# Kernel tuning notes

Measured on AMD Instinct MI355X. Metric: run time of the kernel, lower is better.

The kernel has to match this reference:

```python
import jax, jax.numpy as jnp
import numpy as np

N, NR, NR_SO = 16, 300, 300
C, NUM_REL = 150, 50
D_PRO, D_ROI, D_REL = 512, 12544, 256
K, R, MAX_RECALL, IOU_THRES = 10, 3, 100, 0.5


def _rand_boxes(key, shape):
    # valid (x1,y1,x2,y2) boxes in an ~1000px image
    k1, k2, k3, k4 = jax.random.split(key, 4)
    x1 = jax.random.uniform(k1, shape) * 800.0
    y1 = jax.random.uniform(k2, shape) * 800.0
    w = jax.random.uniform(k3, shape) * 200.0 + 8.0
    h = jax.random.uniform(k4, shape) * 200.0 + 8.0
    return jnp.stack([x1, y1, x1 + w, y1 + h], -1).astype(jnp.float32)


def setup_inputs() -> dict:
    key = jax.random.key(0)
    ks = jax.random.split(key, 12)
    return {
        "auxiliary_rel": jax.random.normal(ks[0], (N, NR, 2 * D_REL), jnp.float32),
        "class_logits": jax.random.normal(ks[1], (N, 2 * NR, C), jnp.float32),
        "pred_bboxes": _rand_boxes(ks[2], (N, 2 * NR)),
        "pro_features": jax.random.normal(ks[3], (N, NR, D_PRO), jnp.float32),
        "roi_features": jax.random.normal(ks[4], (N, NR, D_ROI), jnp.float32),
        "so_class_logits": jax.random.normal(ks[5], (N, NR_SO, 2 * C), jnp.float32),
        "pred_bboxes_so": _rand_boxes(ks[6], (N, 2 * NR_SO)).reshape(N, NR_SO, 8),
        "so_pro_features": jax.random.normal(ks[7], (N, NR_SO, D_PRO), jnp.float32),
        "so_roi_features": jax.random.normal(ks[8], (N, NR_SO, D_ROI), jnp.float32),
        "rel_logits": jax.random.normal(ks[9], (N, NR_SO, NUM_REL), jnp.float32),
        "rel_feat": jax.random.normal(ks[10], (N, NR_SO, D_REL), jnp.float32),
        "vis_table": jnp.zeros((N, NR), dtype=bool),
    }


def _batch_box_iou(b1, b2):
    # b1: [B,N,4], b2: [B,M,4] -> iou [B,N,M] (+1 area convention as in torch src)
    a1 = (b1[..., 3] - b1[..., 1] + 1.0) * (b1[..., 2] - b1[..., 0] + 1.0)
    a2 = (b2[..., 3] - b2[..., 1] + 1.0) * (b2[..., 2] - b2[..., 0] + 1.0)
    lt = jnp.maximum(b1[:, :, None, :2], b2[:, None, :, :2])
    rb = jnp.minimum(b1[:, :, None, 2:], b2[:, None, :, 2:])
    wh = jnp.clip(rb - lt, 0.0)
    inter = wh[..., 0] * wh[..., 1]
    return inter / (a1[:, :, None] + a2[:, None, :] - inter)


def _swap_so(x):
    # swap subject/object halves of the last dim: view (n,k,2,d/2), flip dim 2
    n, k, d = x.shape
    return x.reshape(n, k, 2, d // 2)[:, :, ::-1, :].reshape(n, k, d)


def _forward(auxiliary_rel, class_logits, pred_bboxes, pro_features, roi_features,
             so_class_logits, pred_bboxes_so, so_pro_features, so_roi_features,
             rel_logits, rel_feat, vis_table):
    n = class_logits.shape[0]
    nr = class_logits.shape[1] // 2
    nr_so = so_pro_features.shape[1]
    # ---------- extend_and_select_tri ----------
    probs = jax.nn.sigmoid(so_class_logits).reshape(n, 2 * nr_so, -1)
    boxes = pred_bboxes_so.reshape(n, 2 * nr_so, 4)
    s_score, s_class = jax.lax.top_k(probs[:, 0::2], R)
    o_score, o_class = jax.lax.top_k(probs[:, 1::2], R)
    X, Y = np.meshgrid(np.arange(R), np.arange(R), indexing='ij')
    X, Y = X.ravel(), Y.ravel()
    R2 = R * R
    score_d = jnp.stack([s_score[:, :, X], o_score[:, :, Y]], -1)  # [n,nr_so,R2,2]
    class_d = jnp.stack([s_class[:, :, X], o_class[:, :, Y]], -1)
    sb = jnp.broadcast_to(boxes[:, 0::2][:, :, None, :], (n, nr_so, R2, 4))
    ob = jnp.broadcast_to(boxes[:, 1::2][:, :, None, :], (n, nr_so, R2, 4))
    boxes_d = jnp.stack([sb, ob], 3).reshape(n, nr_so * R2, 8)
    rel_max = jnp.max(jax.nn.sigmoid(rel_logits), -1)  # [n,nr_so]
    triple = (rel_max[:, :, None] * score_d[..., 0] * score_d[..., 1]).reshape(n, nr_so * R2)
    _, tri_idx = jax.lax.top_k(triple, MAX_RECALL)
    tri_idx = jnp.sort(tri_idx, -1)  # boolean-mask gather returns ascending index order
    sel_class = jnp.take_along_axis(class_d.reshape(n, nr_so * R2, 2), tri_idx[..., None], 1).reshape(n, 1, 2 * MAX_RECALL)
    sel_boxes = jnp.take_along_axis(boxes_d, tri_idx[..., None], 1).reshape(n, 2 * MAX_RECALL, 4)
    # ---------- auxiliary_branch (subject slice) ----------
    cls_s = class_logits[:, 0::2, :]
    box_s = pred_bboxes[:, 0::2, :]
    iou_hit = _batch_box_iou(box_s, sel_boxes) >= IOU_THRES  # [n,nr,2*MR]
    pure = jax.nn.sigmoid(cls_s)
    pure_class = jnp.argmax(pure, -1).astype(jnp.int32)  # topk k=1
    cls_eq = pure_class[:, :, None] == sel_class
    is_new = ~jnp.any(iou_hit & cls_eq, -1)  # [n,nr]
    score = jnp.max(pure, -1) - 2.0 * (~is_new) - 2.0 * vis_table
    _, ent_idx = jax.lax.top_k(score, K)
    ent_idx = jnp.sort(ent_idx, -1)
    new_mask = jnp.zeros((n, nr), dtype=bool).at[jnp.arange(n)[:, None], ent_idx].set(True)
    vis_out = vis_table | new_mask
    take = lambda a: jnp.take_along_axis(a, ent_idx[..., None], 1)
    # ---------- assemble auxiliary queries ----------
    aux = take(roi_features)
    so_roi_out = jnp.concatenate([so_roi_features, aux, _swap_so(aux)], 1)
    aux = take(pro_features)
    so_pro_out = jnp.concatenate([so_pro_features, aux, _swap_so(aux)], 1)
    aux = take(pred_bboxes.reshape(n, nr, 8))
    boxes_so_out = jnp.concatenate([pred_bboxes_so, aux, _swap_so(aux)], 1)
    aux = take(class_logits.reshape(n, nr, -1))
    so_cls_out = jnp.concatenate([so_class_logits, aux, _swap_so(aux)], 1)
    aux = take(auxiliary_rel).reshape(n, K, 2, -1)
    rel_out = jnp.concatenate([rel_feat, aux[:, :, 0, :], aux[:, :, 1, :]], 1)
    return so_pro_out, boxes_so_out, so_cls_out, rel_out, so_roi_out, vis_out


def reference(auxiliary_rel, class_logits, pred_bboxes, pro_features, roi_features,
              so_class_logits, pred_bboxes_so, so_pro_features, so_roi_features,
              rel_logits, rel_feat, vis_table):
    return _forward(auxiliary_rel, class_logits, pred_bboxes, pro_features, roi_features,
                    so_class_logits, pred_bboxes_so, so_pro_features, so_roi_features,
                    rel_logits, rel_feat, vis_table)
```

## Files before the change

kernel.cpp:

```cpp
#include <hip/hip_runtime.h>

#pragma clang fp contract(off)

#define NB 16
#define NRR 300
#define KTOP 10

#define OFF_PRO 0
#define OFF_BOX 2621440
#define OFF_CLS 2662400
#define OFF_REL 4198400
#define OFF_ROI 5509120
#define OFF_VIS 69734400

__device__ __forceinline__ float sigm(float x){ return 1.0f/(1.0f + expf(-x)); }

__global__ __launch_bounds__(256) void k_pair(
    const float* __restrict__ so_cls, const float* __restrict__ rel_logits,
    float* __restrict__ s_score, int* __restrict__ s_class,
    float* __restrict__ o_score, int* __restrict__ o_class,
    float* __restrict__ relmax)
{
  int wid  = (blockIdx.x * 256 + threadIdx.x) >> 6;
  int lane = threadIdx.x & 63;
  if (wid >= NB * NRR) return;
  const float* row = so_cls + (size_t)wid * 300;

  for (int half = 0; half < 2; ++half) {
    const float* r = row + half * 150;
    float v[3]; int ci[3];
    #pragma unroll
    for (int j = 0; j < 3; ++j) {
      int c = lane + j * 64;
      ci[j] = c;
      v[j]  = (c < 150) ? r[c] : -1e38f;
    }
    float* ss = half ? o_score : s_score;
    int*   sc = half ? o_class : s_class;
    for (int rd = 0; rd < 3; ++rd) {
      float bv = v[0]; int bi = ci[0];
      if (v[1] > bv) { bv = v[1]; bi = ci[1]; }
      if (v[2] > bv) { bv = v[2]; bi = ci[2]; }
      #pragma unroll
      for (int off = 32; off >= 1; off >>= 1) {
        float ov = __shfl_xor(bv, off, 64);
        int   oi = __shfl_xor(bi, off, 64);
        if (ov > bv || (ov == bv && oi < bi)) { bv = ov; bi = oi; }
      }
      if (lane == 0) { ss[wid*3 + rd] = sigm(bv); sc[wid*3 + rd] = bi; }
      #pragma unroll
      for (int j = 0; j < 3; ++j) if (ci[j] == bi) v[j] = -1e38f;
    }
  }
  float m = (lane < 50) ? rel_logits[(size_t)wid * 50 + lane] : -1e38f;
  #pragma unroll
  for (int off = 32; off >= 1; off >>= 1) m = fmaxf(m, __shfl_xor(m, off, 64));
  if (lane == 0) relmax[wid] = sigm(m);
}

__global__ __launch_bounds__(256) void k_tri100(
    const float* __restrict__ s_score, const int* __restrict__ s_class,
    const float* __restrict__ o_score, const int* __restrict__ o_class,
    const float* __restrict__ relmax,  const float* __restrict__ pbso,
    int* __restrict__ sel_class, float* __restrict__ sel_boxes)
{
  __shared__ unsigned long long keys[4096];
  __shared__ int sidx[128];
  int n = blockIdx.x, tid = threadIdx.x;

  for (int f = tid; f < 4096; f += 256) {
    unsigned long long key = 0ull;
    if (f < 2700) {
      int k = f / 9, p = f - k * 9;
      float s = s_score[(n*NRR + k)*3 + p/3];
      float o = o_score[(n*NRR + k)*3 + (p - (p/3)*3)];
      float v = (relmax[n*NRR + k] * s) * o;
      key = ((unsigned long long)__float_as_uint(v) << 32)
          | (unsigned long long)(0xFFFFFFFFu - (unsigned)f);
    }
    keys[f] = key;
  }
  __syncthreads();
  for (int k = 2; k <= 4096; k <<= 1) {
    for (int j = k >> 1; j > 0; j >>= 1) {
      for (int i = tid; i < 4096; i += 256) {
        int l = i ^ j;
        if (l > i) {
          unsigned long long a = keys[i], b = keys[l];
          bool up = ((i & k) == 0);
          if ((a < b) == up) { keys[i] = b; keys[l] = a; }
        }
      }
      __syncthreads();
    }
  }
  if (tid < 128)
    sidx[tid] = (tid < 100) ? (int)(0xFFFFFFFFu - (unsigned)(keys[tid] & 0xFFFFFFFFull))
                            : 0x7FFFFFFF;
  __syncthreads();
  for (int k = 2; k <= 128; k <<= 1) {
    for (int j = k >> 1; j > 0; j >>= 1) {
      if (tid < 64) {
        for (int i = tid; i < 128; i += 64) {
          int l = i ^ j;
          if (l > i) {
            int a = sidx[i], b = sidx[l];
            bool up = ((i & k) == 0);
            if ((a > b) == up) { sidx[i] = b; sidx[l] = a; }
          }
        }
      }
      __syncthreads();
    }
  }
  if (tid < 200) {
    int m = tid, j = m >> 1, side = m & 1;
    int f = sidx[j];
    int k2 = f / 9, p = f - k2 * 9;
    sel_class[n*200 + m] = side ? o_class[(n*NRR + k2)*3 + (p - (p/3)*3)]
                                : s_class[(n*NRR + k2)*3 + p/3];
    const float4 b = *(const float4*)(pbso + (size_t)(n*NRR + k2)*8 + side*4);
    *(float4*)(sel_boxes + (size_t)(n*200 + m)*4) = b;
  }
}

__global__ __launch_bounds__(256) void k_entity(
    const float* __restrict__ class_logits, const float* __restrict__ pred_bboxes,
    const int* __restrict__ sel_class, const float* __restrict__ sel_boxes,
    const unsigned char* __restrict__ vis, float* __restrict__ score)
{
  int wid  = (blockIdx.x * 256 + threadIdx.x) >> 6;
  int lane = threadIdx.x & 63;
  if (wid >= NB * NRR) return;
  int n = wid / NRR, i = wid - n * NRR;

  const float* r = class_logits + (size_t)(n*600 + 2*i) * 150;
  float bv = r[lane]; int bi = lane;
  for (int c = lane + 64; c < 150; c += 64) {
    float x = r[c];
    if (x > bv) { bv = x; bi = c; }
  }
  #pragma unroll
  for (int off = 32; off >= 1; off >>= 1) {
    float ov = __shfl_xor(bv, off, 64);
    int   oi = __shfl_xor(bi, off, 64);
    if (ov > bv || (ov == bv && oi < bi)) { bv = ov; bi = oi; }
  }
  float maxp = sigm(bv);

  const float* b1 = pred_bboxes + (size_t)(n*600 + 2*i) * 4;
  float x1 = b1[0], y1 = b1[1], x2 = b1[2], y2 = b1[3];
  float a1 = (y2 - y1 + 1.0f) * (x2 - x1 + 1.0f);

  bool hit = false;
  for (int m = lane; m < 200; m += 64) {
    if (sel_class[n*200 + m] == bi) {
      const float4 b2 = *(const float4*)(sel_boxes + (size_t)(n*200 + m)*4);
      float a2 = (b2.w - b2.y + 1.0f) * (b2.z - b2.x + 1.0f);
      float w = fminf(x2, b2.z) - fmaxf(x1, b2.x); if (w < 0.f) w = 0.f;
      float h = fminf(y2, b2.w) - fmaxf(y1, b2.y); if (h < 0.f) h = 0.f;
      float inter = w * h;
      float iou = inter / ((a1 + a2) - inter);
      if (iou >= 0.5f) hit = true;
    }
  }
  bool any = (__ballot(hit) != 0ull);
  if (lane == 0)
    score[wid] = maxp - (any ? 2.0f : 0.0f) - (vis[n*NRR + i] ? 2.0f : 0.0f);
}

__global__ __launch_bounds__(256) void k_top10(
    const float* __restrict__ score, const unsigned char* __restrict__ vis,
    int* __restrict__ ent, float* __restrict__ vis_out)
{
  __shared__ unsigned long long keys[512];
  __shared__ int top[16];
  int n = blockIdx.x, tid = threadIdx.x;

  for (int i = tid; i < 512; i += 256) {
    unsigned long long key = 0ull;
    if (i < NRR) {
      unsigned u = __float_as_uint(score[n*NRR + i]);
      u = (u & 0x80000000u) ? ~u : (u | 0x80000000u);
      key = ((unsigned long long)u << 32)
          | (unsigned long long)(0xFFFFFFFFu - (unsigned)i);
    }
    keys[i] = key;
  }
  __syncthreads();
  for (int k = 2; k <= 512; k <<= 1) {
    for (int j = k >> 1; j > 0; j >>= 1) {
      for (int i = tid; i < 512; i += 256) {
        int l = i ^ j;
        if (l > i) {
          unsigned long long a = keys[i], b = keys[l];
          bool up = ((i & k) == 0);
          if ((a < b) == up) { keys[i] = b; keys[l] = a; }
        }
      }
      __syncthreads();
    }
  }
  if (tid == 0) {
    int tmp[10];
    for (int j = 0; j < 10; ++j)
      tmp[j] = (int)(0xFFFFFFFFu - (unsigned)(keys[j] & 0xFFFFFFFFull));
    for (int a = 1; a < 10; ++a) {
      int x = tmp[a], b = a - 1;
      while (b >= 0 && tmp[b] > x) { tmp[b+1] = tmp[b]; --b; }
      tmp[b+1] = x;
    }
    for (int j = 0; j < 10; ++j) { top[j] = tmp[j]; ent[n*KTOP + j] = tmp[j]; }
  }
  __syncthreads();
  for (int i = tid; i < NRR; i += 256) {
    bool m = vis[n*NRR + i] != 0;
    #pragma unroll
    for (int j = 0; j < 10; ++j) m = m || (top[j] == i);
    vis_out[n*NRR + i] = m ? 1.0f : 0.0f;
  }
}

template <int D, int G, int MODE, typename V>
__global__ __launch_bounds__(256) void k_fuse(
    const V* __restrict__ msrc, const V* __restrict__ gsrc,
    V* __restrict__ dst, const int* __restrict__ ent)
{
  int t = blockIdx.x * 256 + threadIdx.x;
  constexpr int TOT = NB * 320 * D;
  if (t >= TOT) return;
  int bi = t / D, c = t - bi * D;
  int n = bi / 320, row = bi - n * 320;
  V val;
  if (row < 300) {
    val = msrc[(size_t)(n*NRR + row) * D + c];
  } else {
    int e = ent[n*KTOP + (row < 310 ? row - 300 : row - 310)];
    int cc;
    if (row < 310)            cc = c;
    else if (MODE == 0)       cc = (c >= D/2) ? (c - D/2) : (c + D/2);
    else                      cc = D + c;
    val = gsrc[(size_t)(n*NRR + e) * G + cc];
  }
  dst[t] = val;
}

extern "C" void kernel_launch(void* const* d_in, const int* in_sizes, int n_in,
                              void* d_out, int out_size, void* d_ws, size_t ws_size,
                              hipStream_t stream) {
  const float* aux_rel        = (const float*)d_in[0];
  const float* class_logits   = (const float*)d_in[1];
  const float* pred_bboxes    = (const float*)d_in[2];
  const float* pro_features   = (const float*)d_in[3];
  const float* roi_features   = (const float*)d_in[4];
  const float* so_cls         = (const float*)d_in[5];
  const float* pred_bboxes_so = (const float*)d_in[6];
  const float* so_pro         = (const float*)d_in[7];
  const float* so_roi         = (const float*)d_in[8];
  const float* rel_logits     = (const float*)d_in[9];
  const float* rel_feat       = (const float*)d_in[10];
  const unsigned char* vis    = (const unsigned char*)d_in[11];
  float* out = (float*)d_out;

  float* ws        = (float*)d_ws;
  float* s_score   = ws;
  float* o_score   = ws + 14400;
  int*   s_class   = (int*)(ws + 28800);
  int*   o_class   = (int*)(ws + 43200);
  float* relmax    = ws + 57600;
  int*   sel_class = (int*)(ws + 62400);
  float* sel_boxes = ws + 65600;
  float* score     = ws + 78400;
  int*   ent       = (int*)(ws + 83200);

  k_pair  <<<1200, 256, 0, stream>>>(so_cls, rel_logits, s_score, s_class,
                                     o_score, o_class, relmax);
  k_tri100<<<  16, 256, 0, stream>>>(s_score, s_class, o_score, o_class, relmax,
                                     pred_bboxes_so, sel_class, sel_boxes);
  k_entity<<<1200, 256, 0, stream>>>(class_logits, pred_bboxes, sel_class,
                                     sel_boxes, vis, score);
  k_top10 <<<  16, 256, 0, stream>>>(score, vis, ent, out + OFF_VIS);

  k_fuse<128, 128, 0, float4><<< 2560, 256, 0, stream>>>(
      (const float4*)so_pro, (const float4*)pro_features,
      (float4*)(out + OFF_PRO), ent);
  k_fuse<  2,   2, 0, float4><<<   40, 256, 0, stream>>>(
      (const float4*)pred_bboxes_so, (const float4*)pred_bboxes,
      (float4*)(out + OFF_BOX), ent);
  k_fuse<150, 150, 0, float2><<< 3000, 256, 0, stream>>>(
      (const float2*)so_cls, (const float2*)class_logits,
      (float2*)(out + OFF_CLS), ent);
  k_fuse< 64, 128, 1, float4><<< 1280, 256, 0, stream>>>(
      (const float4*)rel_feat, (const float4*)aux_rel,
      (float4*)(out + OFF_REL), ent);
  k_fuse<3136, 3136, 0, float4><<<62720, 256, 0, stream>>>(
      (const float4*)so_roi, (const float4*)roi_features,
      (float4*)(out + OFF_ROI), ent);
}
```

Baseline: 742.8 us.

## Fuse selection pipeline into one kernel overlapped with bulk copies, then gather

Merges the four selection kernels (pair top-3, triplet top-100, entity scoring, top-10) into 16 blocks of a single launch, keeping intermediates in shared memory instead of global workspace. The remaining blocks of that same launch copy the large non-dependent output slices (so_roi, so_pro, so_cls, rel_feat, boxes) with a grid-stride loop, so the bulk memory traffic overlaps the serial selection work. A second kernel then gathers only the 20 dependent rows per image. This cuts launch count and idle time. The cost is that the 16 selection blocks may hold one long critical path while the copy blocks compete for bandwidth.

```diff
diff --git a/kernel.cpp b/kernel.cpp
--- a/kernel.cpp
+++ b/kernel.cpp
@@ -13,68 +13,111 @@
 #define OFF_ROI 5509120
 #define OFF_VIS 69734400
 
+#define OFF_BOX4 655360
+#define OFF_CLS4 665600
+#define OFF_REL4 1049600
+#define OFF_ROI4 1377280
+#define OFF_CLS2 1331200
+
+#define NC 4080
+#define MAIN_TOT 16344000u
+
 __device__ __forceinline__ float sigm(float x){ return 1.0f/(1.0f + expf(-x)); }
 
-__global__ __launch_bounds__(256) void k_pair(
+__global__ __launch_bounds__(512) void k_main(
     const float* __restrict__ so_cls, const float* __restrict__ rel_logits,
-    float* __restrict__ s_score, int* __restrict__ s_class,
-    float* __restrict__ o_score, int* __restrict__ o_class,
-    float* __restrict__ relmax)
-{
-  int wid  = (blockIdx.x * 256 + threadIdx.x) >> 6;
-  int lane = threadIdx.x & 63;
-  if (wid >= NB * NRR) return;
-  const float* row = so_cls + (size_t)wid * 300;
-
-  for (int half = 0; half < 2; ++half) {
-    const float* r = row + half * 150;
-    float v[3]; int ci[3];
-    #pragma unroll
-    for (int j = 0; j < 3; ++j) {
-      int c = lane + j * 64;
-      ci[j] = c;
-      v[j]  = (c < 150) ? r[c] : -1e38f;
-    }
-    float* ss = half ? o_score : s_score;
-    int*   sc = half ? o_class : s_class;
-    for (int rd = 0; rd < 3; ++rd) {
-      float bv = v[0]; int bi = ci[0];
-      if (v[1] > bv) { bv = v[1]; bi = ci[1]; }
-      if (v[2] > bv) { bv = v[2]; bi = ci[2]; }
-      #pragma unroll
-      for (int off = 32; off >= 1; off >>= 1) {
-        float ov = __shfl_xor(bv, off, 64);
-        int   oi = __shfl_xor(bi, off, 64);
-        if (ov > bv || (ov == bv && oi < bi)) { bv = ov; bi = oi; }
-      }
-      if (lane == 0) { ss[wid*3 + rd] = sigm(bv); sc[wid*3 + rd] = bi; }
-      #pragma unroll
-      for (int j = 0; j < 3; ++j) if (ci[j] == bi) v[j] = -1e38f;
-    }
-  }
-  float m = (lane < 50) ? rel_logits[(size_t)wid * 50 + lane] : -1e38f;
-  #pragma unroll
-  for (int off = 32; off >= 1; off >>= 1) m = fmaxf(m, __shfl_xor(m, off, 64));
-  if (lane == 0) relmax[wid] = sigm(m);
-}
-
-__global__ __launch_bounds__(256) void k_tri100(
-    const float* __restrict__ s_score, const int* __restrict__ s_class,
-    const float* __restrict__ o_score, const int* __restrict__ o_class,
-    const float* __restrict__ relmax,  const float* __restrict__ pbso,
-    int* __restrict__ sel_class, float* __restrict__ sel_boxes)
+    const float* __restrict__ class_logits, const float* __restrict__ pred_bboxes,
+    const float* __restrict__ pbso, const unsigned char* __restrict__ vis,
+    const float4* __restrict__ so_roi4, const float4* __restrict__ so_pro4,
+    const float4* __restrict__ so_cls4, const float4* __restrict__ rel_feat4,
+    const float4* __restrict__ pbso4,
+    float* __restrict__ out, float4* __restrict__ out4,
+    int* __restrict__ ent)
 {
   __shared__ unsigned long long keys[4096];
-  __shared__ int sidx[128];
-  int n = blockIdx.x, tid = threadIdx.x;
-
-  for (int f = tid; f < 4096; f += 256) {
+  __shared__ float s_sc[NRR][3], o_sc[NRR][3];
+  __shared__ short s_cl[NRR][3], o_cl[NRR][3];
+  __shared__ float rmax[NRR];
+  __shared__ int   sidx[128];
+  __shared__ int   selc[200];
+  __shared__ float selb[200][4];
+  __shared__ float escore[NRR];
+  __shared__ int   entl[16];
+
+  const int tid = threadIdx.x;
+
+  if (blockIdx.x >= 16) {
+    unsigned gtid   = (blockIdx.x - 16) * 512u + (unsigned)tid;
+    unsigned stride = (gridDim.x - 16) * 512u;
+    for (unsigned i = gtid; i < MAIN_TOT; i += stride) {
+      if (i < 15052800u) {
+        unsigned n = i / 940800u, c = i - n*940800u;
+        out4[OFF_ROI4 + n*1003520u + c] = so_roi4[n*940800u + c];
+      } else if (i < 15667200u) {
+        unsigned j = i - 15052800u;
+        unsigned n = j / 38400u, c = j - n*38400u;
+        out4[n*40960u + c] = so_pro4[n*38400u + c];
+      } else if (i < 16027200u) {
+        unsigned j = i - 15667200u;
+        unsigned n = j / 22500u, c = j - n*22500u;
+        out4[OFF_CLS4 + n*24000u + c] = so_cls4[n*22500u + c];
+      } else if (i < 16334400u) {
+        unsigned j = i - 16027200u;
+        unsigned n = j / 19200u, c = j - n*19200u;
+        out4[OFF_REL4 + n*20480u + c] = rel_feat4[n*19200u + c];
+      } else {
+        unsigned j = i - 16334400u;
+        unsigned n = j / 600u, c = j - n*600u;
+        out4[OFF_BOX4 + n*640u + c] = pbso4[n*600u + c];
+      }
+    }
+    return;
+  }
+
+  const int n = blockIdx.x;
+  const int w = tid >> 6, lane = tid & 63;
+
+  for (int k = w; k < NRR; k += 8) {
+    const float* row = so_cls + (size_t)(n*NRR + k) * 300;
+    for (int half = 0; half < 2; ++half) {
+      const float* r = row + half * 150;
+      float v[3]; int ci[3];
+      #pragma unroll
+      for (int j = 0; j < 3; ++j) {
+        int c = lane + j * 64;
+        ci[j] = c;
+        v[j]  = (c < 150) ? r[c] : -1e38f;
+      }
+      for (int rd = 0; rd < 3; ++rd) {
+        float bv = v[0]; int bi = ci[0];
+        if (v[1] > bv) { bv = v[1]; bi = ci[1]; }
+        if (v[2] > bv) { bv = v[2]; bi = ci[2]; }
+        #pragma unroll
+        for (int off = 32; off >= 1; off >>= 1) {
+          float ov = __shfl_xor(bv, off, 64);
+          int   oi = __shfl_xor(bi, off, 64);
+          if (ov > bv || (ov == bv && oi < bi)) { bv = ov; bi = oi; }
+        }
+        if (lane == 0) {
+          if (half) { o_sc[k][rd] = sigm(bv); o_cl[k][rd] = (short)bi; }
+          else      { s_sc[k][rd] = sigm(bv); s_cl[k][rd] = (short)bi; }
+        }
+        #pragma unroll
+        for (int j = 0; j < 3; ++j) if (ci[j] == bi) v[j] = -1e38f;
+      }
+    }
+    float m = (lane < 50) ? rel_logits[(size_t)(n*NRR + k)*50 + lane] : -1e38f;
+    #pragma unroll
+    for (int off = 32; off >= 1; off >>= 1) m = fmaxf(m, __shfl_xor(m, off, 64));
+    if (lane == 0) rmax[k] = sigm(m);
+  }
+  __syncthreads();
+
+  for (int f = tid; f < 4096; f += 512) {
     unsigned long long key = 0ull;
     if (f < 2700) {
       int k = f / 9, p = f - k * 9;
-      float s = s_score[(n*NRR + k)*3 + p/3];
-      float o = o_score[(n*NRR + k)*3 + (p - (p/3)*3)];
-      float v = (relmax[n*NRR + k] * s) * o;
+      float v = (rmax[k] * s_sc[k][p/3]) * o_sc[k][p - (p/3)*3];
       key = ((unsigned long long)__float_as_uint(v) << 32)
           | (unsigned long long)(0xFFFFFFFFu - (unsigned)f);
     }
@@ -83,7 +126,7 @@
   __syncthreads();
   for (int k = 2; k <= 4096; k <<= 1) {
     for (int j = k >> 1; j > 0; j >>= 1) {
-      for (int i = tid; i < 4096; i += 256) {
+      for (int i = tid; i < 4096; i += 512) {
         int l = i ^ j;
         if (l > i) {
           unsigned long long a = keys[i], b = keys[l];
@@ -94,6 +137,7 @@
       __syncthreads();
     }
   }
+
   if (tid < 128)
     sidx[tid] = (tid < 100) ? (int)(0xFFFFFFFFu - (unsigned)(keys[tid] & 0xFFFFFFFFull))
                             : 0x7FFFFFFF;
@@ -114,84 +158,66 @@
     }
   }
   if (tid < 200) {
-    int m = tid, j = m >> 1, side = m & 1;
-    int f = sidx[j];
+    int m = tid, j2 = m >> 1, side = m & 1;
+    int f = sidx[j2];
     int k2 = f / 9, p = f - k2 * 9;
-    sel_class[n*200 + m] = side ? o_class[(n*NRR + k2)*3 + (p - (p/3)*3)]
-                                : s_class[(n*NRR + k2)*3 + p/3];
+    selc[m] = side ? (int)o_cl[k2][p - (p/3)*3] : (int)s_cl[k2][p/3];
     const float4 b = *(const float4*)(pbso + (size_t)(n*NRR + k2)*8 + side*4);
-    *(float4*)(sel_boxes + (size_t)(n*200 + m)*4) = b;
-  }
-}
-
-__global__ __launch_bounds__(256) void k_entity(
-    const float* __restrict__ class_logits, const float* __restrict__ pred_bboxes,
-    const int* __restrict__ sel_class, const float* __restrict__ sel_boxes,
-    const unsigned char* __restrict__ vis, float* __restrict__ score)
-{
-  int wid  = (blockIdx.x * 256 + threadIdx.x) >> 6;
-  int lane = threadIdx.x & 63;
-  if (wid >= NB * NRR) return;
-  int n = wid / NRR, i = wid - n * NRR;
-
-  const float* r = class_logits + (size_t)(n*600 + 2*i) * 150;
-  float bv = r[lane]; int bi = lane;
-  for (int c = lane + 64; c < 150; c += 64) {
-    float x = r[c];
-    if (x > bv) { bv = x; bi = c; }
-  }
-  #pragma unroll
-  for (int off = 32; off >= 1; off >>= 1) {
-    float ov = __shfl_xor(bv, off, 64);
-    int   oi = __shfl_xor(bi, off, 64);
-    if (ov > bv || (ov == bv && oi < bi)) { bv = ov; bi = oi; }
-  }
-  float maxp = sigm(bv);
-
-  const float* b1 = pred_bboxes + (size_t)(n*600 + 2*i) * 4;
-  float x1 = b1[0], y1 = b1[1], x2 = b1[2], y2 = b1[3];
-  float a1 = (y2 - y1 + 1.0f) * (x2 - x1 + 1.0f);
-
-  bool hit = false;
-  for (int m = lane; m < 200; m += 64) {
-    if (sel_class[n*200 + m] == bi) {
-      const float4 b2 = *(const float4*)(sel_boxes + (size_t)(n*200 + m)*4);
-      float a2 = (b2.w - b2.y + 1.0f) * (b2.z - b2.x + 1.0f);
-      float w = fminf(x2, b2.z) - fmaxf(x1, b2.x); if (w < 0.f) w = 0.f;
-      float h = fminf(y2, b2.w) - fmaxf(y1, b2.y); if (h < 0.f) h = 0.f;
-      float inter = w * h;
-      float iou = inter / ((a1 + a2) - inter);
-      if (iou >= 0.5f) hit = true;
-    }
-  }
-  bool any = (__ballot(hit) != 0ull);
-  if (lane == 0)
-    score[wid] = maxp - (any ? 2.0f : 0.0f) - (vis[n*NRR + i] ? 2.0f : 0.0f);
-}
-
-__global__ __launch_bounds__(256) void k_top10(
-    const float* __restrict__ score, const unsigned char* __restrict__ vis,
-    int* __restrict__ ent, float* __restrict__ vis_out)
-{
-  __shared__ unsigned long long keys[512];
-  __shared__ int top[16];
-  int n = blockIdx.x, tid = threadIdx.x;
-
-  for (int i = tid; i < 512; i += 256) {
+    selb[m][0] = b.x; selb[m][1] = b.y; selb[m][2] = b.z; selb[m][3] = b.w;
+  }
+  __syncthreads();
+
+  for (int i = w; i < NRR; i += 8) {
+    const float* r = class_logits + (size_t)(n*600 + 2*i) * 150;
+    float bv = r[lane]; int bi = lane;
+    for (int c = lane + 64; c < 150; c += 64) {
+      float x = r[c];
+      if (x > bv) { bv = x; bi = c; }
+    }
+    #pragma unroll
+    for (int off = 32; off >= 1; off >>= 1) {
+      float ov = __shfl_xor(bv, off, 64);
+      int   oi = __shfl_xor(bi, off, 64);
+      if (ov > bv || (ov == bv && oi < bi)) { bv = ov; bi = oi; }
+    }
+    float maxp = sigm(bv);
+
+    const float* b1 = pred_bboxes + (size_t)(n*600 + 2*i) * 4;
+    float x1 = b1[0], y1 = b1[1], x2 = b1[2], y2 = b1[3];
+    float a1 = (y2 - y1 + 1.0f) * (x2 - x1 + 1.0f);
+
+    bool hit = false;
+    for (int m = lane; m < 200; m += 64) {
+      if (selc[m] == bi) {
+        float a2 = (selb[m][3] - selb[m][1] + 1.0f) * (selb[m][2] - selb[m][0] + 1.0f);
+        float ww = fminf(x2, selb[m][2]) - fmaxf(x1, selb[m][0]); if (ww < 0.f) ww = 0.f;
+        float hh = fminf(y2, selb[m][3]) - fmaxf(y1, selb[m][1]); if (hh < 0.f) hh = 0.f;
+        float inter = ww * hh;
+        float iou = inter / ((a1 + a2) - inter);
+        if (iou >= 0.5f) hit = true;
+      }
+    }
+    bool any = (__ballot(hit) != 0ull);
+    if (lane == 0)
+      escore[i] = maxp - (any ? 2.0f : 0.0f) - (vis[n*NRR + i] ? 2.0f : 0.0f);
+  }
+  __syncthreads();
+
+  {
     unsigned long long key = 0ull;
-    if (i < NRR) {
-      unsigned u = __float_as_uint(score[n*NRR + i]);
+    if (tid < NRR) {
+      unsigned u = __float_as_uint(escore[tid]);
       u = (u & 0x80000000u) ? ~u : (u | 0x80000000u);
       key = ((unsigned long long)u << 32)
-          | (unsigned long long)(0xFFFFFFFFu - (unsigned)i);
-    }
-    keys[i] = key;
+          | (unsigned long long)(0xFFFFFFFFu - (unsigned)tid);
+    }
+    keys[tid] = key;
   }
   __syncthreads();
   for (int k = 2; k <= 512; k <<= 1) {
     for (int j = k >> 1; j > 0; j >>= 1) {
-      for (int i = tid; i < 512; i += 256) {
-        int l = i ^ j;
+      {
+        int i = tid, l = i ^ j;
         if (l > i) {
           unsigned long long a = keys[i], b = keys[l];
           bool up = ((i & k) == 0);
@@ -210,39 +236,66 @@
       while (b >= 0 && tmp[b] > x) { tmp[b+1] = tmp[b]; --b; }
       tmp[b+1] = x;
     }
-    for (int j = 0; j < 10; ++j) { top[j] = tmp[j]; ent[n*KTOP + j] = tmp[j]; }
-  }
-  __syncthreads();
-  for (int i = tid; i < NRR; i += 256) {
+    for (int j = 0; j < 10; ++j) { entl[j] = tmp[j]; ent[n*KTOP + j] = tmp[j]; }
+  }
+  __syncthreads();
+  for (int i = tid; i < NRR; i += 512) {
     bool m = vis[n*NRR + i] != 0;
     #pragma unroll
-    for (int j = 0; j < 10; ++j) m = m || (top[j] == i);
-    vis_out[n*NRR + i] = m ? 1.0f : 0.0f;
+    for (int j = 0; j < 10; ++j) m = m || (entl[j] == i);
+    out[OFF_VIS + n*NRR + i] = m ? 1.0f : 0.0f;
   }
 }
 
-template <int D, int G, int MODE, typename V>
-__global__ __launch_bounds__(256) void k_fuse(
-    const V* __restrict__ msrc, const V* __restrict__ gsrc,
-    V* __restrict__ dst, const int* __restrict__ ent)
+__global__ __launch_bounds__(256) void k_gather(
+    const float4* __restrict__ roi4, const float4* __restrict__ pro4,
+    const float4* __restrict__ aux4, const float4* __restrict__ cls4,
+    const float2* __restrict__ cls2, const float4* __restrict__ box4,
+    float4* __restrict__ out4, float2* __restrict__ out2,
+    const int* __restrict__ ent)
 {
-  int t = blockIdx.x * 256 + threadIdx.x;
-  constexpr int TOT = NB * 320 * D;
-  if (t >= TOT) return;
-  int bi = t / D, c = t - bi * D;
-  int n = bi / 320, row = bi - n * 320;
-  V val;
-  if (row < 300) {
-    val = msrc[(size_t)(n*NRR + row) * D + c];
-  } else {
-    int e = ent[n*KTOP + (row < 310 ? row - 300 : row - 310)];
-    int cc;
-    if (row < 310)            cc = c;
-    else if (MODE == 0)       cc = (c >= D/2) ? (c - D/2) : (c + D/2);
-    else                      cc = D + c;
-    val = gsrc[(size_t)(n*NRR + e) * G + cc];
-  }
-  dst[t] = val;
+  unsigned t = blockIdx.x * 256u + threadIdx.x;
+  if (t < 1003520u) {
+    unsigned n = t / 62720u, rem = t - n*62720u;
+    unsigned r = rem / 3136u, c = rem - r*3136u;
+    int e = ent[n*KTOP + (r < 10u ? r : r - 10u)];
+    unsigned cc = (r < 10u) ? c : (c >= 1568u ? c - 1568u : c + 1568u);
+    out4[OFF_ROI4 + (n*320u + 300u + r)*3136u + c] = roi4[(n*300u + (unsigned)e)*3136u + cc];
+  } else if (t < 1044480u) {
+    unsigned j = t - 1003520u;
+    unsigned n = j / 2560u, rem = j - n*2560u;
+    unsigned r = rem / 128u, c = rem - r*128u;
+    int e = ent[n*KTOP + (r < 10u ? r : r - 10u)];
+    unsigned cc = (r < 10u) ? c : (c >= 64u ? c - 64u : c + 64u);
+    out4[(n*320u + 300u + r)*128u + c] = pro4[(n*300u + (unsigned)e)*128u + cc];
+  } else if (t < 1064960u) {
+    unsigned j = t - 1044480u;
+    unsigned n = j / 1280u, rem = j - n*1280u;
+    unsigned r = rem / 64u, c = rem - r*64u;
+    int e = ent[n*KTOP + (r < 10u ? r : r - 10u)];
+    unsigned cc = (r < 10u) ? c : 64u + c;
+    out4[OFF_REL4 + (n*320u + 300u + r)*64u + c] = aux4[(n*300u + (unsigned)e)*128u + cc];
+  } else if (t < 1076960u) {
+    unsigned j = t - 1064960u;
+    unsigned n = j / 750u, rem = j - n*750u;
+    unsigned r = rem / 75u, c = rem - r*75u;
+    int e = ent[n*KTOP + r];
+    out4[OFF_CLS4 + (n*320u + 300u + r)*75u + c] = cls4[(n*300u + (unsigned)e)*75u + c];
+  } else if (t < 1100960u) {
+    unsigned j = t - 1076960u;
+    unsigned n = j / 1500u, rem = j - n*1500u;
+    unsigned r = rem / 150u, c = rem - r*150u;
+    int e = ent[n*KTOP + r];
+    unsigned cc = (c >= 75u) ? c - 75u : c + 75u;
+    out2[OFF_CLS2 + (n*320u + 310u + r)*150u + c] = cls2[(n*300u + (unsigned)e)*150u + cc];
+  } else if (t < 1101600u) {
+    unsigned j = t - 1100960u;
+    unsigned n = j / 40u, rem = j - n*40u;
+    unsigned r = rem / 2u, c = rem & 1u;
+    int e = ent[n*KTOP + (r < 10u ? r : r - 10u)];
+    unsigned cc = (r < 10u) ? c : (c ^ 1u);
+    out4[OFF_BOX4 + (n*320u + 300u + r)*2u + c] = box4[(n*300u + (unsigned)e)*2u + cc];
+  }
 }
 
 extern "C" void kernel_launch(void* const* d_in, const int* in_sizes, int n_in,
@@ -261,39 +314,17 @@
   const float* rel_feat       = (const float*)d_in[10];
   const unsigned char* vis    = (const unsigned char*)d_in[11];
   float* out = (float*)d_out;
-
-  float* ws        = (float*)d_ws;
-  float* s_score   = ws;
-  float* o_score   = ws + 14400;
-  int*   s_class   = (int*)(ws + 28800);
-  int*   o_class   = (int*)(ws + 43200);
-  float* relmax    = ws + 57600;
-  int*   sel_class = (int*)(ws + 62400);
-  float* sel_boxes = ws + 65600;
-  float* score     = ws + 78400;
-  int*   ent       = (int*)(ws + 83200);
-
-  k_pair  <<<1200, 256, 0, stream>>>(so_cls, rel_logits, s_score, s_class,
-                                     o_score, o_class, relmax);
-  k_tri100<<<  16, 256, 0, stream>>>(s_score, s_class, o_score, o_class, relmax,
-                                     pred_bboxes_so, sel_class, sel_boxes);
-  k_entity<<<1200, 256, 0, stream>>>(class_logits, pred_bboxes, sel_class,
-                                     sel_boxes, vis, score);
-  k_top10 <<<  16, 256, 0, stream>>>(score, vis, ent, out + OFF_VIS);
-
-  k_fuse<128, 128, 0, float4><<< 2560, 256, 0, stream>>>(
-      (const float4*)so_pro, (const float4*)pro_features,
-      (float4*)(out + OFF_PRO), ent);
-  k_fuse<  2,   2, 0, float4><<<   40, 256, 0, stream>>>(
-      (const float4*)pred_bboxes_so, (const float4*)pred_bboxes,
-      (float4*)(out + OFF_BOX), ent);
-  k_fuse<150, 150, 0, float2><<< 3000, 256, 0, stream>>>(
-      (const float2*)so_cls, (const float2*)class_logits,
-      (float2*)(out + OFF_CLS), ent);
-  k_fuse< 64, 128, 1, float4><<< 1280, 256, 0, stream>>>(
-      (const float4*)rel_feat, (const float4*)aux_rel,
-      (float4*)(out + OFF_REL), ent);
-  k_fuse<3136, 3136, 0, float4><<<62720, 256, 0, stream>>>(
-      (const float4*)so_roi, (const float4*)roi_features,
-      (float4*)(out + OFF_ROI), ent);
+  int*   ent = (int*)d_ws;
+
+  k_main<<<16 + NC, 512, 0, stream>>>(
+      so_cls, rel_logits, class_logits, pred_bboxes, pred_bboxes_so, vis,
+      (const float4*)so_roi, (const float4*)so_pro, (const float4*)so_cls,
+      (const float4*)rel_feat, (const float4*)pred_bboxes_so,
+      out, (float4*)out, ent);
+
+  k_gather<<<4304, 256, 0, stream>>>(
+      (const float4*)roi_features, (const float4*)pro_features,
+      (const float4*)aux_rel, (const float4*)class_logits,
+      (const float2*)class_logits, (const float4*)pred_bboxes,
+      (float4*)out, (float2*)out, ent);
 }
```

After: 918.0 us. 1.24x slower.
